# Optimization experiments

Measured on AMD Instinct MI355X. Metric: run time of the kernel, lower is better.

## Reference

```python
import jax, jax.numpy as jnp
import numpy as np

B, N, P = 256, 32, 32
OBS, ACT = 96, 32
OBS_P, ACT_P = 96, 32
DIN = OBS + ACT          # obs_act_input_dim = 128
DOUT = 128               # obs_act_output_dim
DIN_P = OBS_P + ACT_P    # obs_act_input_dim_people = 128
DOUT_P = 128             # obs_act_output_dim_people
DF1, DF2 = 64, 32        # final hidden / final_output_dim


def setup_inputs() -> dict:
    key = jax.random.key(0)
    ks = jax.random.split(key, 13)
    s = 0.05
    return {
        "states": jax.random.normal(ks[0], (B, N, OBS), jnp.float32),
        "policies": jax.random.uniform(ks[1], (B, N, ACT), jnp.float32),
        "actions": jax.random.uniform(ks[2], (B, N, ACT), jnp.float32),
        "states_people": jax.random.normal(ks[3], (B, P, OBS_P), jnp.float32),
        "actions_people": jax.random.uniform(ks[4], (B, P, ACT_P), jnp.float32),
        "W_k": jax.random.normal(ks[5], (DIN, DOUT), jnp.float32) * s,
        "W_q": jax.random.normal(ks[6], (DIN, DOUT), jnp.float32) * s,
        "W_v": jax.random.normal(ks[7], (DIN, DOUT), jnp.float32) * s,
        "W_kp": jax.random.normal(ks[8], (DIN_P, DOUT_P), jnp.float32) * s,
        "W_qp": jax.random.normal(ks[9], (DIN, DOUT), jnp.float32) * s,
        "W_vp": jax.random.normal(ks[10], (DIN_P, DOUT_P), jnp.float32) * s,
        "W_f1": jax.random.normal(ks[11], (DOUT + DOUT_P, DF1), jnp.float32) * s,
        "W_f2": jax.random.normal(ks[12], (DF1, DF2), jnp.float32) * s,
    }


def reference(states, policies, actions, states_people, actions_people,
              W_k, W_q, W_v, W_kp, W_qp, W_vp, W_f1, W_f2):
    n = states.shape[1]
    p = states_people.shape[1]
    dk = jnp.asarray(W_k.shape[1], states.dtype)
    dkp = jnp.asarray(W_kp.shape[1], states.dtype)

    oa = jnp.concatenate([states, actions], axis=-1)    # [B,N,DIN]
    op = jnp.concatenate([states, policies], axis=-1)   # [B,N,DIN]

    k = oa @ W_k   # [B,N,DOUT]
    q = oa @ W_q   # [B,N,DOUT]
    scores = jnp.einsum('bid,bjd->bij', q, k)            # [B,N,N]
    # torch path: transpose then softmax over last axis of transposed scores
    weight = jax.nn.softmax(jnp.swapaxes(scores, 1, 2) / jnp.sqrt(dk), axis=-1)  # [B,N,N]

    # place_policies/place_actions masks == identity selector over (i==j)
    eye = jnp.eye(n, dtype=oa.dtype)[None, :, :, None]   # [1,N,N,1]
    oap = eye * op[:, None, :, :] + (1.0 - eye) * oa[:, None, :, :]  # [B,N,N,DIN]
    av = jnp.tanh(oap @ W_v)                             # [B,N,N,DOUT]
    # torch: mean_j( av[b,i,j] * weight[b,a,j] ) -> [B,N(a),N(i),DOUT]
    wav = jnp.einsum('baj,bijd->baid', weight, av) / n

    oa_p = jnp.concatenate([states_people, actions_people], axis=-1)  # [B,P,DIN_P]
    kp = oa_p @ W_kp                                     # [B,P,DOUT_P]
    qp = oa @ W_qp                                       # [B,N,DOUT_P]
    avp = jnp.tanh(oa_p @ W_vp)                          # [B,P,DOUT_P]
    scores_p = jnp.einsum('bnd,bpd->bnp', qp, kp)        # [B,N,P]
    # original softmax over dim=-2 (agents)
    wp = jax.nn.softmax(scores_p / jnp.sqrt(dkp), axis=-2)           # [B,N,P]
    wavp = jnp.einsum('bnp,bpd->bnd', wp, avp) / p       # mean over people

    wavp_b = jnp.broadcast_to(wavp[:, :, None, :], wav.shape[:3] + (wavp.shape[-1],))
    node_features = jnp.concatenate([wav, wavp_b], axis=-1)          # [B,N,N,256]

    h = jax.nn.leaky_relu(node_features @ W_f1)          # slope 0.01 (torch default)
    value = h @ W_f2                                     # [B,N,N,DF2]
    return value, weight, wp[..., None]
```

## Files before the change

kernel.cpp:

```cpp
#include <hip/hip_runtime.h>
#include <math.h>

#define VAL_SZ  (256*32*32*32)
#define W_OFF   VAL_SZ
#define WP_OFF  (VAL_SZ + 256*32*32)

#define PK_WV   0
#define PK_WVP  16384
#define PK_MQ   32768
#define PK_MP   49152
#define PK_WF1  65536
#define PK_WF2  81920

typedef short  bf16x8 __attribute__((ext_vector_type(8)));
typedef float  f32x4  __attribute__((ext_vector_type(4)));

#define MFMA(a, b, c) __builtin_amdgcn_mfma_f32_16x16x32_bf16(a, b, c, 0, 0, 0)

static __device__ __forceinline__ unsigned short f2bf(float f) {
    union { float f; unsigned u; } v; v.f = f;
    unsigned r = (v.u + 0x7FFF + ((v.u >> 16) & 1)) >> 16;
    return (unsigned short)r;
}

static __device__ __forceinline__ float fast_tanh(float x) {
    x = fminf(fmaxf(x, -12.0f), 12.0f);
    float e = __expf(2.0f * x);
    return (e - 1.0f) / (e + 1.0f);
}

static __device__ __forceinline__ bf16x8 afrag(const unsigned short* Mb, int stride,
                                               int row0, int kt) {
    int lane = threadIdx.x & 63;
    return *(const bf16x8*)(Mb + (row0 + (lane & 15)) * stride + kt * 32 + (lane >> 4) * 8);
}

static __device__ __forceinline__ bf16x8 bfrag_pk(const unsigned short* base, int NT,
                                                  int kt, int nt) {
    int lane = threadIdx.x & 63;
    return *(const bf16x8*)(base + (((kt * NT + nt) * 64) + lane) * 8);
}

__global__ __launch_bounds__(256) void pack_weights(
    const float* __restrict__ Wq, const float* __restrict__ Wk,
    const float* __restrict__ Wv, const float* __restrict__ Wkp,
    const float* __restrict__ Wqp, const float* __restrict__ Wvp,
    const float* __restrict__ Wf1, const float* __restrict__ Wf2,
    unsigned short* __restrict__ pk)
{
    const float scale = 0.08838834764831845f;
    if (blockIdx.x < 24) {
        int pid = blockIdx.x * 256 + threadIdx.x;
        int sub = pid >> 11;
        int r = pid & 2047;
        int lane = r & 63;
        int l16 = lane & 15, quad = lane >> 4;
        union { unsigned short u[8]; bf16x8 v; } o;
        if (sub < 2) {
            const float* W = (sub == 0) ? Wv : Wvp;
            int ktnt = r >> 6;
            int n = (ktnt & 7) * 16 + l16;
            int kb = (ktnt >> 3) * 32 + quad * 8;
#pragma unroll
            for (int j = 0; j < 8; ++j) o.u[j] = f2bf(W[(kb + j) * 128 + n]);
            *(bf16x8*)(pk + ((sub == 0) ? PK_WV : PK_WVP) + (ktnt * 64 + lane) * 8) = o.v;
        } else {
            int ktnt = r >> 6;
            int n = (ktnt & 3) * 16 + l16;
            int kb = (ktnt >> 2) * 32 + quad * 8;
#pragma unroll
            for (int j = 0; j < 8; ++j) o.u[j] = f2bf(Wf1[(kb + j) * 64 + n]);
            *(bf16x8*)(pk + PK_WF1 + (ktnt * 64 + lane) * 8) = o.v;
        }
    } else if (blockIdx.x == 24) {
        int r = threadIdx.x;
        int lane = r & 63;
        int l16 = lane & 15, quad = lane >> 4;
        int ktnt = r >> 6;
        int n = (ktnt & 1) * 16 + l16;
        int kb = (ktnt >> 1) * 32 + quad * 8;
        union { unsigned short u[8]; bf16x8 v; } o;
#pragma unroll
        for (int j = 0; j < 8; ++j) o.u[j] = f2bf(Wf2[(kb + j) * 32 + n]);
        *(bf16x8*)(pk + PK_WF2 + (ktnt * 64 + lane) * 8) = o.v;
    } else {
        int mid = (blockIdx.x - 25) * 256 + threadIdx.x;
        int mat = mid >> 14;
        int idx = mid & 16383;
        int k = idx >> 7, n = idx & 127;
        const float* A  = (mat == 0) ? Wq : Wqp;
        const float* Bm = (mat == 0) ? Wk : Wkp;
        const float4* a4 = (const float4*)(A + k * 128);
        const float4* b4 = (const float4*)(Bm + n * 128);
        float acc = 0.f;
#pragma unroll 8
        for (int c = 0; c < 32; ++c) {
            float4 x = a4[c], y = b4[c];
            acc = fmaf(x.x, y.x, acc);
            acc = fmaf(x.y, y.y, acc);
            acc = fmaf(x.z, y.z, acc);
            acc = fmaf(x.w, y.w, acc);
        }
        int kt = k >> 5, quad = (k >> 3) & 3, j = k & 7;
        int nt = n >> 4, l16 = n & 15;
        pk[((mat == 0) ? PK_MQ : PK_MP)
           + ((kt * 8 + nt) * 64 + quad * 16 + l16) * 8 + j] = f2bf(acc * scale);
    }
}

__global__ __launch_bounds__(1024) void critic_A(
    const float* __restrict__ states, const float* __restrict__ policies,
    const float* __restrict__ actions, const float* __restrict__ states_p,
    const float* __restrict__ actions_p,
    const unsigned short* __restrict__ pk, float* __restrict__ out)
{
    __shared__ __align__(16) unsigned char SM[63744];
    unsigned short* OA  = (unsigned short*)(SM + 0);
    unsigned short* OP  = (unsigned short*)(SM + 8704);
    unsigned short* NF  = (unsigned short*)(SM + 0);
    unsigned short* VT  = (unsigned short*)(SM + 17408);
    unsigned short* TD  = (unsigned short*)(SM + 27648);
    float*          FP  = (float*)(SM + 27648);
    unsigned short* TL  = (unsigned short*)(SM + 37888);
    unsigned short* WB1 = (unsigned short*)(SM + 37888);
    unsigned short* WB2 = (unsigned short*)(SM + 40448);
    unsigned short* TPL = (unsigned short*)(SM + 46592);
    float*          GP  = (float*)(SM + 46592);
    float*          SC1 = (float*)(SM + 55296);
    float*          SC2 = (float*)(SM + 59520);

    const int tid = threadIdx.x;
    const int b = blockIdx.x;
    const int lane = tid & 63, wv = tid >> 6;
    const int l16 = lane & 15, quad = lane >> 4;
    const float invN = 1.0f / 32.0f;
    const f32x4 Z = {0.f, 0.f, 0.f, 0.f};

    {
        const float* st = states   + (size_t)b * 3072;
        const float* ac = actions  + (size_t)b * 1024;
        const float* po = policies + (size_t)b * 1024;
#pragma unroll
        for (int k = 0; k < 4; ++k) {
            int idx = tid + k * 1024;
            int n = idx >> 7, d = idx & 127;
            float sv, pv;
            if (d < 96) { sv = st[n * 96 + d]; pv = sv; }
            else        { sv = ac[n * 32 + d - 96]; pv = po[n * 32 + d - 96]; }
            OA[n * 136 + d] = f2bf(sv);
            OP[n * 136 + d] = f2bf(pv);
        }
    }
    __syncthreads();

    if (wv < 8) {
        int mt = wv & 1, ntA = wv >> 1, ntB = ntA + 4;
        f32x4 va0 = Z, va1 = Z, vp0 = Z, vp1 = Z;
#pragma unroll
        for (int kt = 0; kt < 4; ++kt) {
            bf16x8 aA = afrag(OA, 136, mt * 16, kt);
            bf16x8 aP = afrag(OP, 136, mt * 16, kt);
            bf16x8 b0 = bfrag_pk(pk + PK_WV, 8, kt, ntA);
            bf16x8 b1 = bfrag_pk(pk + PK_WV, 8, kt, ntB);
            va0 = MFMA(aA, b0, va0); va1 = MFMA(aA, b1, va1);
            vp0 = MFMA(aP, b0, vp0); vp1 = MFMA(aP, b1, vp1);
        }
#pragma unroll
        for (int r = 0; r < 4; ++r) {
            int row = mt * 16 + quad * 4 + r;
            float tva0 = fast_tanh(va0[r]), tvp0 = fast_tanh(vp0[r]);
            float tva1 = fast_tanh(va1[r]), tvp1 = fast_tanh(vp1[r]);
            VT[(ntA * 16 + l16) * 40 + row] = f2bf(tva0);
            VT[(ntB * 16 + l16) * 40 + row] = f2bf(tva1);
            TD[row * 136 + ntA * 16 + l16] = f2bf(tvp0 - tva0);
            TD[row * 136 + ntB * 16 + l16] = f2bf(tvp1 - tva1);
        }
    } else {
        int q = wv - 8;
        int q4 = q & 3;
        int mt = q4 & 1, ntb = q4 >> 1;
        const unsigned short* pkM = pk + ((q < 4) ? PK_MQ : PK_MP);
        unsigned short* outT = (q < 4) ? TL : TPL;
        bf16x8 afr[4];
#pragma unroll
        for (int kt = 0; kt < 4; ++kt) afr[kt] = afrag(OA, 136, mt * 16, kt);
#pragma unroll
        for (int t4 = 0; t4 < 4; ++t4) {
            int nt = ntb + t4 * 2;
            f32x4 acc = Z;
#pragma unroll
            for (int kt = 0; kt < 4; ++kt)
                acc = MFMA(afr[kt], bfrag_pk(pkM, 8, kt, nt), acc);
#pragma unroll
            for (int r = 0; r < 4; ++r)
                outT[(mt * 16 + quad * 4 + r) * 136 + nt * 16 + l16] = f2bf(acc[r]);
        }
    }
    __syncthreads();

    f32x4 gReg = Z;
    int gmt = 0, gnt = 0;
    if (wv < 8) {
        gmt = wv & 1; gnt = wv >> 1;
#pragma unroll
        for (int kt = 0; kt < 4; ++kt)
            gReg = MFMA(afrag(TD, 136, gmt * 16, kt), bfrag_pk(pk + PK_WF1, 4, kt, gnt), gReg);
    } else {
        const float* st = states_p  + (size_t)b * 3072;
        const float* ac = actions_p + (size_t)b * 1024;
        int t512 = tid - 512;
#pragma unroll
        for (int k = 0; k < 8; ++k) {
            int idx = t512 + k * 512;
            int n = idx >> 7, d = idx & 127;
            OP[n * 136 + d] = f2bf((d < 96) ? st[n * 96 + d] : ac[n * 32 + d - 96]);
        }
    }
    __syncthreads();

    if (wv < 8) {
        int sp = wv >> 2;
        int w4 = wv & 3;
        int mt = w4 & 1, nt = w4 >> 1;
        const unsigned short* Am = sp ? TPL : TL;
        const unsigned short* Bm = sp ? OP : OA;
        float* SC = sp ? SC2 : SC1;
        f32x4 acc = Z;
#pragma unroll
        for (int kt = 0; kt < 4; ++kt)
            acc = MFMA(afrag(Am, 136, mt * 16, kt), afrag(Bm, 136, nt * 16, kt), acc);
#pragma unroll
        for (int r = 0; r < 4; ++r)
            SC[(mt * 16 + quad * 4 + r) * 33 + nt * 16 + l16] = acc[r];
    } else {
        int q = wv - 8;
        int mt = q & 1, ntA = q >> 1, ntB = ntA + 4;
        f32x4 a0 = Z, a1 = Z;
#pragma unroll
        for (int kt = 0; kt < 4; ++kt) {
            bf16x8 a = afrag(OP, 136, mt * 16, kt);
            a0 = MFMA(a, bfrag_pk(pk + PK_WVP, 8, kt, ntA), a0);
            a1 = MFMA(a, bfrag_pk(pk + PK_WVP, 8, kt, ntB), a1);
        }
#pragma unroll
        for (int r = 0; r < 4; ++r) {
            int row = mt * 16 + quad * 4 + r;
            TD[(ntA * 16 + l16) * 40 + row] = f2bf(fast_tanh(a0[r]));
            TD[(ntB * 16 + l16) * 40 + row] = f2bf(fast_tanh(a1[r]));
        }
    }
    __syncthreads();

    {
        int j = tid & 31, a = (tid >> 5) & 31;
        float x = SC1[j * 33 + a];
        float m = x;
#pragma unroll
        for (int msk = 16; msk >= 1; msk >>= 1) m = fmaxf(m, __shfl_xor(m, msk));
        float e = __expf(x - m);
        float s = e;
#pragma unroll
        for (int msk = 16; msk >= 1; msk >>= 1) s += __shfl_xor(s, msk);
        float w = e / s;
        out[W_OFF + (size_t)b * 1024 + a * 32 + j] = w;
        WB1[a * 40 + j] = f2bf(w);
        SC1[j * 33 + a] = w;

        int n = tid & 31, p = (tid >> 5) & 31;
        float x2 = SC2[n * 33 + p];
        float m2 = x2;
#pragma unroll
        for (int msk = 16; msk >= 1; msk >>= 1) m2 = fmaxf(m2, __shfl_xor(m2, msk));
        float e2 = __expf(x2 - m2);
        float s2 = e2;
#pragma unroll
        for (int msk = 16; msk >= 1; msk >>= 1) s2 += __shfl_xor(s2, msk);
        float w2 = e2 / s2;
        out[WP_OFF + (size_t)b * 1024 + n * 32 + p] = w2;
        WB2[n * 40 + p] = f2bf(w2);
    }
    __syncthreads();

    {
        int mt = wv & 1, nt = wv >> 1;
        f32x4 s = MFMA(afrag(WB1, 40, mt * 16, 0), afrag(VT, 40, nt * 16, 0), Z);
        f32x4 wvp = MFMA(afrag(WB2, 40, mt * 16, 0), afrag(TD, 40, nt * 16, 0), Z);
#pragma unroll
        for (int r = 0; r < 4; ++r) {
            int row = mt * 16 + quad * 4 + r;
            NF[row * 264 + nt * 16 + l16]       = f2bf(s[r] * invN);
            NF[row * 264 + 128 + nt * 16 + l16] = f2bf(wvp[r] * invN);
        }
    }
    __syncthreads();

    if (wv < 8) {
        int mt = wv & 1, nt = wv >> 1;
        f32x4 f = Z;
#pragma unroll
        for (int kt = 0; kt < 8; ++kt)
            f = MFMA(afrag(NF, 264, mt * 16, kt), bfrag_pk(pk + PK_WF1, 4, kt, nt), f);
#pragma unroll
        for (int r = 0; r < 4; ++r) {
            FP[(mt * 16 + quad * 4 + r) * 66 + nt * 16 + l16] = f[r];
            GP[(gmt * 16 + quad * 4 + r) * 67 + gnt * 16 + l16] = gReg[r];
        }
    }
    __syncthreads();

    {
        bf16x8 bw[2][2];
#pragma unroll
        for (int kt = 0; kt < 2; ++kt)
#pragma unroll
            for (int nt = 0; nt < 2; ++nt)
                bw[kt][nt] = bfrag_pk(pk + PK_WF2, 2, kt, nt);

#pragma unroll
        for (int t4 = 0; t4 < 4; ++t4) {
            int tile = wv + t4 * 16;
            int m0 = tile * 16;
            int a = m0 >> 5;
            int i = (m0 & 31) + l16;
            float w = SC1[i * 33 + a] * invN;
            const float* Fa = FP + a * 66;
            const float* Gi = GP + i * 67;
            f32x4 acc0 = Z, acc1 = Z;
#pragma unroll
            for (int kt = 0; kt < 2; ++kt) {
                union { unsigned short u[8]; bf16x8 v; } h;
                int dbase = kt * 32 + quad * 8;
#pragma unroll
                for (int j = 0; j < 8; ++j) {
                    float z = fmaf(w, Gi[dbase + j], Fa[dbase + j]);
                    z = fmaxf(z, 0.01f * z);
                    h.u[j] = f2bf(z);
                }
                acc0 = MFMA(h.v, bw[kt][0], acc0);
                acc1 = MFMA(h.v, bw[kt][1], acc1);
            }
            float* base = out + (size_t)b * 32768 + (size_t)m0 * 32;
#pragma unroll
            for (int r = 0; r < 4; ++r) {
                int row = quad * 4 + r;
                base[row * 32 + l16]      = acc0[r];
                base[row * 32 + 16 + l16] = acc1[r];
            }
        }
    }
}

extern "C" void kernel_launch(void* const* d_in, const int* in_sizes, int n_in,
                              void* d_out, int out_size, void* d_ws, size_t ws_size,
                              hipStream_t stream)
{
    const float* states    = (const float*)d_in[0];
    const float* policies  = (const float*)d_in[1];
    const float* actions   = (const float*)d_in[2];
    const float* states_p  = (const float*)d_in[3];
    const float* actions_p = (const float*)d_in[4];
    const float* Wk        = (const float*)d_in[5];
    const float* Wq        = (const float*)d_in[6];
    const float* Wv        = (const float*)d_in[7];
    const float* Wkp       = (const float*)d_in[8];
    const float* Wqp       = (const float*)d_in[9];
    const float* Wvp       = (const float*)d_in[10];
    const float* Wf1       = (const float*)d_in[11];
    const float* Wf2       = (const float*)d_in[12];
    float* out = (float*)d_out;
    unsigned short* pk = (unsigned short*)d_ws;

    pack_weights<<<153, 256, 0, stream>>>(Wq, Wk, Wv, Wkp, Wqp, Wvp, Wf1, Wf2, pk);
    critic_A<<<256, 1024, 0, stream>>>(states, policies, actions,
                                       states_p, actions_p, pk, out);
}
```

Before: 112.3 us.

## Fuse weight packing into main kernel and compute Q/K projections directly

Drops the separate weight-packing kernel. Each block now gathers fp32 weights and converts them to bf16 MFMA fragments on the fly. The precomputed Wq·Wk^T product is replaced by explicit Q and K projections whose scores are computed per block, and the shared-memory layout and stage schedule are reorganised around this. The goal is to remove a kernel launch and its dependency, at the cost of redundant strided global gathers and extra MFMA work in every block. Softmax inputs are now stored as bf16 before scaling, which slightly reduces precision.

```diff
diff --git a/kernel.cpp b/kernel.cpp
--- a/kernel.cpp
+++ b/kernel.cpp
@@ -1,16 +1,8 @@
 #include <hip/hip_runtime.h>
-#include <math.h>
 
 #define VAL_SZ  (256*32*32*32)
 #define W_OFF   VAL_SZ
 #define WP_OFF  (VAL_SZ + 256*32*32)
-
-#define PK_WV   0
-#define PK_WVP  16384
-#define PK_MQ   32768
-#define PK_MP   49152
-#define PK_WF1  65536
-#define PK_WF2  81920
 
 typedef short  bf16x8 __attribute__((ext_vector_type(8)));
 typedef float  f32x4  __attribute__((ext_vector_type(4)));
@@ -22,7 +14,10 @@
     unsigned r = (v.u + 0x7FFF + ((v.u >> 16) & 1)) >> 16;
     return (unsigned short)r;
 }
-
+static __device__ __forceinline__ float bf2f(unsigned short u) {
+    union { unsigned u; float f; } v; v.u = ((unsigned)u) << 16;
+    return v.f;
+}
 static __device__ __forceinline__ float fast_tanh(float x) {
     x = fminf(fmaxf(x, -12.0f), 12.0f);
     float e = __expf(2.0f * x);
@@ -35,105 +30,48 @@
     return *(const bf16x8*)(Mb + (row0 + (lane & 15)) * stride + kt * 32 + (lane >> 4) * 8);
 }
 
-static __device__ __forceinline__ bf16x8 bfrag_pk(const unsigned short* base, int NT,
-                                                  int kt, int nt) {
+static __device__ __forceinline__ bf16x8 bfrag_gather(const float* __restrict__ W,
+                                                      int ldn, int kt, int nt) {
     int lane = threadIdx.x & 63;
-    return *(const bf16x8*)(base + (((kt * NT + nt) * 64) + lane) * 8);
-}
-
-__global__ __launch_bounds__(256) void pack_weights(
-    const float* __restrict__ Wq, const float* __restrict__ Wk,
+    int l16 = lane & 15, quad = lane >> 4;
+    const float* p = W + (kt * 32 + quad * 8) * ldn + nt * 16 + l16;
+    union { unsigned short u[8]; bf16x8 v; } o;
+#pragma unroll
+    for (int j = 0; j < 8; ++j) o.u[j] = f2bf(p[j * ldn]);
+    return o.v;
+}
+
+__global__ __launch_bounds__(1024) void critic_fused(
+    const float* __restrict__ states, const float* __restrict__ policies,
+    const float* __restrict__ actions, const float* __restrict__ states_p,
+    const float* __restrict__ actions_p,
+    const float* __restrict__ Wk, const float* __restrict__ Wq,
     const float* __restrict__ Wv, const float* __restrict__ Wkp,
     const float* __restrict__ Wqp, const float* __restrict__ Wvp,
     const float* __restrict__ Wf1, const float* __restrict__ Wf2,
-    unsigned short* __restrict__ pk)
+    float* __restrict__ out)
 {
-    const float scale = 0.08838834764831845f;
-    if (blockIdx.x < 24) {
-        int pid = blockIdx.x * 256 + threadIdx.x;
-        int sub = pid >> 11;
-        int r = pid & 2047;
-        int lane = r & 63;
-        int l16 = lane & 15, quad = lane >> 4;
-        union { unsigned short u[8]; bf16x8 v; } o;
-        if (sub < 2) {
-            const float* W = (sub == 0) ? Wv : Wvp;
-            int ktnt = r >> 6;
-            int n = (ktnt & 7) * 16 + l16;
-            int kb = (ktnt >> 3) * 32 + quad * 8;
-#pragma unroll
-            for (int j = 0; j < 8; ++j) o.u[j] = f2bf(W[(kb + j) * 128 + n]);
-            *(bf16x8*)(pk + ((sub == 0) ? PK_WV : PK_WVP) + (ktnt * 64 + lane) * 8) = o.v;
-        } else {
-            int ktnt = r >> 6;
-            int n = (ktnt & 3) * 16 + l16;
-            int kb = (ktnt >> 2) * 32 + quad * 8;
-#pragma unroll
-            for (int j = 0; j < 8; ++j) o.u[j] = f2bf(Wf1[(kb + j) * 64 + n]);
-            *(bf16x8*)(pk + PK_WF1 + (ktnt * 64 + lane) * 8) = o.v;
-        }
-    } else if (blockIdx.x == 24) {
-        int r = threadIdx.x;
-        int lane = r & 63;
-        int l16 = lane & 15, quad = lane >> 4;
-        int ktnt = r >> 6;
-        int n = (ktnt & 1) * 16 + l16;
-        int kb = (ktnt >> 1) * 32 + quad * 8;
-        union { unsigned short u[8]; bf16x8 v; } o;
-#pragma unroll
-        for (int j = 0; j < 8; ++j) o.u[j] = f2bf(Wf2[(kb + j) * 32 + n]);
-        *(bf16x8*)(pk + PK_WF2 + (ktnt * 64 + lane) * 8) = o.v;
-    } else {
-        int mid = (blockIdx.x - 25) * 256 + threadIdx.x;
-        int mat = mid >> 14;
-        int idx = mid & 16383;
-        int k = idx >> 7, n = idx & 127;
-        const float* A  = (mat == 0) ? Wq : Wqp;
-        const float* Bm = (mat == 0) ? Wk : Wkp;
-        const float4* a4 = (const float4*)(A + k * 128);
-        const float4* b4 = (const float4*)(Bm + n * 128);
-        float acc = 0.f;
-#pragma unroll 8
-        for (int c = 0; c < 32; ++c) {
-            float4 x = a4[c], y = b4[c];
-            acc = fmaf(x.x, y.x, acc);
-            acc = fmaf(x.y, y.y, acc);
-            acc = fmaf(x.z, y.z, acc);
-            acc = fmaf(x.w, y.w, acc);
-        }
-        int kt = k >> 5, quad = (k >> 3) & 3, j = k & 7;
-        int nt = n >> 4, l16 = n & 15;
-        pk[((mat == 0) ? PK_MQ : PK_MP)
-           + ((kt * 8 + nt) * 64 + quad * 16 + l16) * 8 + j] = f2bf(acc * scale);
-    }
-}
-
-__global__ __launch_bounds__(1024) void critic_A(
-    const float* __restrict__ states, const float* __restrict__ policies,
-    const float* __restrict__ actions, const float* __restrict__ states_p,
-    const float* __restrict__ actions_p,
-    const unsigned short* __restrict__ pk, float* __restrict__ out)
-{
-    __shared__ __align__(16) unsigned char SM[63744];
+    __shared__ __align__(16) unsigned char SM[64000];
     unsigned short* OA  = (unsigned short*)(SM + 0);
-    unsigned short* OP  = (unsigned short*)(SM + 8704);
+    unsigned short* TD  = (unsigned short*)(SM + 8704);
     unsigned short* NF  = (unsigned short*)(SM + 0);
-    unsigned short* VT  = (unsigned short*)(SM + 17408);
-    unsigned short* TD  = (unsigned short*)(SM + 27648);
-    float*          FP  = (float*)(SM + 27648);
-    unsigned short* TL  = (unsigned short*)(SM + 37888);
-    unsigned short* WB1 = (unsigned short*)(SM + 37888);
-    unsigned short* WB2 = (unsigned short*)(SM + 40448);
-    unsigned short* TPL = (unsigned short*)(SM + 46592);
-    float*          GP  = (float*)(SM + 46592);
-    float*          SC1 = (float*)(SM + 55296);
-    float*          SC2 = (float*)(SM + 59520);
+    unsigned short* OP  = (unsigned short*)(SM + 17408);
+    unsigned short* QL  = (unsigned short*)(SM + 26112);
+    unsigned short* WPB = (unsigned short*)(SM + 26112);
+    float*          FP  = (float*)(SM + 26112);
+    unsigned short* KL  = (unsigned short*)(SM + 34816);
+    float*          GP  = (float*)(SM + 34816);
+    unsigned short* VT  = (unsigned short*)(SM + 43520);
+    unsigned short* AVT = (unsigned short*)(SM + 51712);
+    unsigned short* SB1 = (unsigned short*)(SM + 59904);
+    unsigned short* SB2 = (unsigned short*)(SM + 61952);
 
     const int tid = threadIdx.x;
     const int b = blockIdx.x;
     const int lane = tid & 63, wv = tid >> 6;
     const int l16 = lane & 15, quad = lane >> 4;
     const float invN = 1.0f / 32.0f;
+    const float scale = 0.08838834764831845f;
     const f32x4 Z = {0.f, 0.f, 0.f, 0.f};
 
     {
@@ -160,8 +98,8 @@
         for (int kt = 0; kt < 4; ++kt) {
             bf16x8 aA = afrag(OA, 136, mt * 16, kt);
             bf16x8 aP = afrag(OP, 136, mt * 16, kt);
-            bf16x8 b0 = bfrag_pk(pk + PK_WV, 8, kt, ntA);
-            bf16x8 b1 = bfrag_pk(pk + PK_WV, 8, kt, ntB);
+            bf16x8 b0 = bfrag_gather(Wv, 128, kt, ntA);
+            bf16x8 b1 = bfrag_gather(Wv, 128, kt, ntB);
             va0 = MFMA(aA, b0, va0); va1 = MFMA(aA, b1, va1);
             vp0 = MFMA(aP, b0, vp0); vp1 = MFMA(aP, b1, vp1);
         }
@@ -170,30 +108,32 @@
             int row = mt * 16 + quad * 4 + r;
             float tva0 = fast_tanh(va0[r]), tvp0 = fast_tanh(vp0[r]);
             float tva1 = fast_tanh(va1[r]), tvp1 = fast_tanh(vp1[r]);
-            VT[(ntA * 16 + l16) * 40 + row] = f2bf(tva0);
-            VT[(ntB * 16 + l16) * 40 + row] = f2bf(tva1);
+            VT[(ntA * 16 + l16) * 32 + row] = f2bf(tva0);
+            VT[(ntB * 16 + l16) * 32 + row] = f2bf(tva1);
             TD[row * 136 + ntA * 16 + l16] = f2bf(tvp0 - tva0);
             TD[row * 136 + ntB * 16 + l16] = f2bf(tvp1 - tva1);
         }
     } else {
-        int q = wv - 8;
-        int q4 = q & 3;
-        int mt = q4 & 1, ntb = q4 >> 1;
-        const unsigned short* pkM = pk + ((q < 4) ? PK_MQ : PK_MP);
-        unsigned short* outT = (q < 4) ? TL : TPL;
+        int s = wv - 8;
+        int mt = s & 1, pb2 = s >> 1;
         bf16x8 afr[4];
 #pragma unroll
         for (int kt = 0; kt < 4; ++kt) afr[kt] = afrag(OA, 136, mt * 16, kt);
 #pragma unroll
-        for (int t4 = 0; t4 < 4; ++t4) {
-            int nt = ntb + t4 * 2;
-            f32x4 acc = Z;
-#pragma unroll
-            for (int kt = 0; kt < 4; ++kt)
-                acc = MFMA(afr[kt], bfrag_pk(pkM, 8, kt, nt), acc);
-#pragma unroll
-            for (int r = 0; r < 4; ++r)
-                outT[(mt * 16 + quad * 4 + r) * 136 + nt * 16 + l16] = f2bf(acc[r]);
+        for (int m2 = 0; m2 < 2; ++m2) {
+            const float* W = m2 ? Wk : Wq;
+            unsigned short* dst = m2 ? KL : QL;
+#pragma unroll
+            for (int h = 0; h < 2; ++h) {
+                int nt = pb2 + h * 4;
+                f32x4 acc = Z;
+#pragma unroll
+                for (int kt = 0; kt < 4; ++kt)
+                    acc = MFMA(afr[kt], bfrag_gather(W, 128, kt, nt), acc);
+#pragma unroll
+                for (int r = 0; r < 4; ++r)
+                    dst[(mt * 16 + quad * 4 + r) * 136 + nt * 16 + l16] = f2bf(acc[r]);
+            }
         }
     }
     __syncthreads();
@@ -204,92 +144,124 @@
         gmt = wv & 1; gnt = wv >> 1;
 #pragma unroll
         for (int kt = 0; kt < 4; ++kt)
-            gReg = MFMA(afrag(TD, 136, gmt * 16, kt), bfrag_pk(pk + PK_WF1, 4, kt, gnt), gReg);
+            gReg = MFMA(afrag(TD, 136, gmt * 16, kt), bfrag_gather(Wf1, 64, kt, gnt), gReg);
+    } else if (wv < 12) {
+        int s = wv - 8;
+        int mt = s & 1, nt = s >> 1;
+        f32x4 acc = Z;
+#pragma unroll
+        for (int kt = 0; kt < 4; ++kt)
+            acc = MFMA(afrag(QL, 136, mt * 16, kt), afrag(KL, 136, nt * 16, kt), acc);
+#pragma unroll
+        for (int r = 0; r < 4; ++r)
+            SB1[(nt * 16 + l16) * 32 + mt * 16 + quad * 4 + r] = f2bf(acc[r]);
     } else {
         const float* st = states_p  + (size_t)b * 3072;
         const float* ac = actions_p + (size_t)b * 1024;
-        int t512 = tid - 512;
-#pragma unroll
-        for (int k = 0; k < 8; ++k) {
-            int idx = t512 + k * 512;
+        int t256 = tid - 768;
+#pragma unroll
+        for (int k = 0; k < 16; ++k) {
+            int idx = t256 + k * 256;
             int n = idx >> 7, d = idx & 127;
             OP[n * 136 + d] = f2bf((d < 96) ? st[n * 96 + d] : ac[n * 32 + d - 96]);
         }
     }
     __syncthreads();
 
-    if (wv < 8) {
-        int sp = wv >> 2;
-        int w4 = wv & 3;
-        int mt = w4 & 1, nt = w4 >> 1;
-        const unsigned short* Am = sp ? TPL : TL;
-        const unsigned short* Bm = sp ? OP : OA;
-        float* SC = sp ? SC2 : SC1;
-        f32x4 acc = Z;
-#pragma unroll
-        for (int kt = 0; kt < 4; ++kt)
-            acc = MFMA(afrag(Am, 136, mt * 16, kt), afrag(Bm, 136, nt * 16, kt), acc);
-#pragma unroll
-        for (int r = 0; r < 4; ++r)
-            SC[(mt * 16 + quad * 4 + r) * 33 + nt * 16 + l16] = acc[r];
-    } else {
-        int q = wv - 8;
-        int mt = q & 1, ntA = q >> 1, ntB = ntA + 4;
-        f32x4 a0 = Z, a1 = Z;
-#pragma unroll
-        for (int kt = 0; kt < 4; ++kt) {
-            bf16x8 a = afrag(OP, 136, mt * 16, kt);
-            a0 = MFMA(a, bfrag_pk(pk + PK_WVP, 8, kt, ntA), a0);
-            a1 = MFMA(a, bfrag_pk(pk + PK_WVP, 8, kt, ntB), a1);
-        }
-#pragma unroll
-        for (int r = 0; r < 4; ++r) {
-            int row = mt * 16 + quad * 4 + r;
-            TD[(ntA * 16 + l16) * 40 + row] = f2bf(fast_tanh(a0[r]));
-            TD[(ntB * 16 + l16) * 40 + row] = f2bf(fast_tanh(a1[r]));
-        }
-    }
-    __syncthreads();
-
-    {
-        int j = tid & 31, a = (tid >> 5) & 31;
-        float x = SC1[j * 33 + a];
-        float m = x;
-#pragma unroll
-        for (int msk = 16; msk >= 1; msk >>= 1) m = fmaxf(m, __shfl_xor(m, msk));
-        float e = __expf(x - m);
-        float s = e;
-#pragma unroll
-        for (int msk = 16; msk >= 1; msk >>= 1) s += __shfl_xor(s, msk);
-        float w = e / s;
-        out[W_OFF + (size_t)b * 1024 + a * 32 + j] = w;
-        WB1[a * 40 + j] = f2bf(w);
-        SC1[j * 33 + a] = w;
-
-        int n = tid & 31, p = (tid >> 5) & 31;
-        float x2 = SC2[n * 33 + p];
-        float m2 = x2;
-#pragma unroll
-        for (int msk = 16; msk >= 1; msk >>= 1) m2 = fmaxf(m2, __shfl_xor(m2, msk));
-        float e2 = __expf(x2 - m2);
-        float s2 = e2;
-#pragma unroll
-        for (int msk = 16; msk >= 1; msk >>= 1) s2 += __shfl_xor(s2, msk);
-        float w2 = e2 / s2;
-        out[WP_OFF + (size_t)b * 1024 + n * 32 + p] = w2;
-        WB2[n * 40 + p] = f2bf(w2);
-    }
-    __syncthreads();
-
     {
         int mt = wv & 1, nt = wv >> 1;
-        f32x4 s = MFMA(afrag(WB1, 40, mt * 16, 0), afrag(VT, 40, nt * 16, 0), Z);
-        f32x4 wvp = MFMA(afrag(WB2, 40, mt * 16, 0), afrag(TD, 40, nt * 16, 0), Z);
+        bf16x8 ao[4], ap[4];
+#pragma unroll
+        for (int kt = 0; kt < 4; ++kt) {
+            ao[kt] = afrag(OA, 136, mt * 16, kt);
+            ap[kt] = afrag(OP, 136, mt * 16, kt);
+        }
+        f32x4 aq = Z, akp = Z, aav = Z;
+#pragma unroll
+        for (int kt = 0; kt < 4; ++kt) {
+            aq  = MFMA(ao[kt], bfrag_gather(Wqp, 128, kt, nt), aq);
+            akp = MFMA(ap[kt], bfrag_gather(Wkp, 128, kt, nt), akp);
+            aav = MFMA(ap[kt], bfrag_gather(Wvp, 128, kt, nt), aav);
+        }
 #pragma unroll
         for (int r = 0; r < 4; ++r) {
             int row = mt * 16 + quad * 4 + r;
-            NF[row * 264 + nt * 16 + l16]       = f2bf(s[r] * invN);
-            NF[row * 264 + 128 + nt * 16 + l16] = f2bf(wvp[r] * invN);
+            QL[row * 136 + nt * 16 + l16] = f2bf(aq[r]);
+            KL[row * 136 + nt * 16 + l16] = f2bf(akp[r]);
+            AVT[(nt * 16 + l16) * 32 + row] = f2bf(fast_tanh(aav[r]));
+        }
+    }
+    __syncthreads();
+
+    if (wv < 4) {
+        int mt = wv & 1, nt = wv >> 1;
+        f32x4 acc = Z;
+#pragma unroll
+        for (int kt = 0; kt < 4; ++kt)
+            acc = MFMA(afrag(QL, 136, mt * 16, kt), afrag(KL, 136, nt * 16, kt), acc);
+#pragma unroll
+        for (int r = 0; r < 4; ++r)
+            SB2[(nt * 16 + l16) * 32 + mt * 16 + quad * 4 + r] = f2bf(acc[r]);
+    } else if (wv >= 8) {
+        int t512 = tid - 512;
+#pragma unroll
+        for (int rep = 0; rep < 2; ++rep) {
+            int idx = t512 + rep * 512;
+            int j = idx & 31, a = idx >> 5;
+            float x = bf2f(SB1[a * 32 + j]) * scale;
+            float m = x;
+#pragma unroll
+            for (int msk = 16; msk >= 1; msk >>= 1) m = fmaxf(m, __shfl_xor(m, msk));
+            float e = __expf(x - m);
+            float s = e;
+#pragma unroll
+            for (int msk = 16; msk >= 1; msk >>= 1) s += __shfl_xor(s, msk);
+            float w = e / s;
+            out[W_OFF + (size_t)b * 1024 + a * 32 + j] = w;
+            SB1[a * 32 + j] = f2bf(w);
+        }
+    }
+    __syncthreads();
+
+    if (wv < 8) {
+#pragma unroll
+        for (int rep = 0; rep < 2; ++rep) {
+            int idx = tid + rep * 512;
+            int n = idx & 31, p = idx >> 5;
+            float x = bf2f(SB2[p * 32 + n]) * scale;
+            float m = x;
+#pragma unroll
+            for (int msk = 16; msk >= 1; msk >>= 1) m = fmaxf(m, __shfl_xor(m, msk));
+            float e = __expf(x - m);
+            float s = e;
+#pragma unroll
+            for (int msk = 16; msk >= 1; msk >>= 1) s += __shfl_xor(s, msk);
+            float w2 = e / s;
+            out[WP_OFF + (size_t)b * 1024 + n * 32 + p] = w2;
+            WPB[n * 32 + p] = f2bf(w2);
+        }
+    } else {
+        int s = wv - 8;
+        int mt = s & 1, nt0 = s >> 1, nt1 = nt0 + 4;
+        bf16x8 aw = afrag(SB1, 32, mt * 16, 0);
+        f32x4 s0 = MFMA(aw, afrag(VT, 32, nt0 * 16, 0), Z);
+        f32x4 s1 = MFMA(aw, afrag(VT, 32, nt1 * 16, 0), Z);
+#pragma unroll
+        for (int r = 0; r < 4; ++r) {
+            int row = mt * 16 + quad * 4 + r;
+            NF[row * 264 + nt0 * 16 + l16] = f2bf(s0[r] * invN);
+            NF[row * 264 + nt1 * 16 + l16] = f2bf(s1[r] * invN);
+        }
+    }
+    __syncthreads();
+
+    {
+        int mt = wv & 1, nt = wv >> 1;
+        f32x4 acc = MFMA(afrag(WPB, 32, mt * 16, 0), afrag(AVT, 32, nt * 16, 0), Z);
+#pragma unroll
+        for (int r = 0; r < 4; ++r) {
+            int row = mt * 16 + quad * 4 + r;
+            NF[row * 264 + 128 + nt * 16 + l16] = f2bf(acc[r] * invN);
         }
     }
     __syncthreads();
@@ -299,7 +271,7 @@
         f32x4 f = Z;
 #pragma unroll
         for (int kt = 0; kt < 8; ++kt)
-            f = MFMA(afrag(NF, 264, mt * 16, kt), bfrag_pk(pk + PK_WF1, 4, kt, nt), f);
+            f = MFMA(afrag(NF, 264, mt * 16, kt), bfrag_gather(Wf1, 64, kt, nt), f);
 #pragma unroll
         for (int r = 0; r < 4; ++r) {
             FP[(mt * 16 + quad * 4 + r) * 66 + nt * 16 + l16] = f[r];
@@ -314,7 +286,7 @@
         for (int kt = 0; kt < 2; ++kt)
 #pragma unroll
             for (int nt = 0; nt < 2; ++nt)
-                bw[kt][nt] = bfrag_pk(pk + PK_WF2, 2, kt, nt);
+                bw[kt][nt] = bfrag_gather(Wf2, 32, kt, nt);
 
 #pragma unroll
         for (int t4 = 0; t4 < 4; ++t4) {
@@ -322,7 +294,7 @@
             int m0 = tile * 16;
             int a = m0 >> 5;
             int i = (m0 & 31) + l16;
-            float w = SC1[i * 33 + a] * invN;
+            float w = bf2f(SB1[a * 32 + i]) * invN;
             const float* Fa = FP + a * 66;
             const float* Gi = GP + i * 67;
             f32x4 acc0 = Z, acc1 = Z;
@@ -368,9 +340,9 @@
     const float* Wf1       = (const float*)d_in[11];
     const float* Wf2       = (const float*)d_in[12];
     float* out = (float*)d_out;
-    unsigned short* pk = (unsigned short*)d_ws;
-
-    pack_weights<<<153, 256, 0, stream>>>(Wq, Wk, Wv, Wkp, Wqp, Wvp, Wf1, Wf2, pk);
-    critic_A<<<256, 1024, 0, stream>>>(states, policies, actions,
-                                       states_p, actions_p, pk, out);
-}
+
+    critic_fused<<<256, 1024, 0, stream>>>(states, policies, actions,
+                                           states_p, actions_p,
+                                           Wk, Wq, Wv, Wkp, Wqp, Wvp,
+                                           Wf1, Wf2, out);
+}
```

Result: slower. 115.1 us (+2.5%).
